# Optimization experiments

Hardware: AMD Instinct MI355X
Metric: run time of the kernel (lower is better)

Reference implementation:

```python
import jax, jax.numpy as jnp
import numpy as np

N = 4096      # num_nodes
F = 256       # node_dim
K = 4         # num_heads
FP = 64       # out_dim per head
P_EDGE = 0.008  # edge probability (~33 avg degree)


def setup_inputs() -> dict:
    key = jax.random.key(0)
    k1, k2, k3, k4, k5 = jax.random.split(key, 5)
    x = jax.random.normal(k1, (N, F), dtype=jnp.float32)
    # binary adjacency mask with self loops so every row has a neighbor
    adj = (jax.random.uniform(k2, (N, N)) < P_EDGE).astype(jnp.float32)
    mask = jnp.maximum(adj, jnp.eye(N, dtype=jnp.float32))
    batch = jnp.zeros((N,), dtype=jnp.int32)  # unused (is_final_layer=False)
    # xavier-style init for W (node_dim -> K*FP) and attention vectors
    w_scale = np.sqrt(2.0 / (F + K * FP)).astype(np.float32)
    W = jax.random.normal(k3, (F, K * FP), dtype=jnp.float32) * w_scale
    b = jnp.zeros((K * FP,), dtype=jnp.float32)
    a_scale = np.sqrt(2.0 / (K * FP + 1)).astype(np.float32)
    a_left = jax.random.normal(k4, (1, K, FP), dtype=jnp.float32) * a_scale
    a_right = jax.random.normal(k5, (1, K, FP), dtype=jnp.float32) * a_scale
    return {"x": x, "mask": mask, "batch": batch, "W": W, "b": b,
            "a_left": a_left, "a_right": a_right}


def reference(x, mask, batch, W, b, a_left, a_right):
    # dropout prob = 0.0 (eval mode) -> identity
    x_proj = (x @ W + b).reshape(N, K, FP)                 # (N,K,F')
    score_src = (x_proj * a_left).sum(axis=-1)             # (N,K)
    score_tgt = (x_proj * a_right).sum(axis=-1)            # (N,K)
    score = score_src[:, None, :] + score_tgt[None, :, :]  # (N,N,K)
    score = jax.nn.leaky_relu(score, negative_slope=0.2)
    # non-standard global mean/std normalization (torch .std() is unbiased)
    score = (score - score.mean()) / score.std(ddof=1)
    score = jnp.exp(score)
    m = mask[:, :, None]                                   # (N,N,1)
    denom = (score * m).sum(axis=1, keepdims=True)         # (N,1,K)
    aij = (score / denom) * m                              # (N,N,K)
    attention = jnp.transpose(aij, (2, 0, 1))              # (K,N,N)
    h_prime = jnp.einsum('knm,mkf->nkf', attention, x_proj)  # (N,K,F')
    h_prime = jax.nn.elu(h_prime)
    # is_final_layer=False -> concat heads
    return h_prime.reshape(N, K * FP)
```

## Files before the change

kernel.cpp:

```cpp
#include <hip/hip_runtime.h>
#include <hip/hip_bf16.h>
#include <math.h>

#define NN 4096
#define FF 256
#define KH 4
#define FP 64
#define NCOL 256
#define MAXNBR 512
#define MOM_BLOCKS 2048

__device__ __forceinline__ float bits2f(unsigned b) {
    union { unsigned u; float f; } c; c.u = b << 16; return c.f;
}
__device__ __forceinline__ int is_fp32(const void* mask) {
    return ((const unsigned*)mask)[0] == 0x3F800000u;
}

#define OFF_SUMS   0
#define OFF_PART   128
#define OFF_XP     65536
#define OFF_SRC    4259840
#define OFF_TGT    4325376

__global__ __launch_bounds__(256) void gat_gemm_valu(
        const void* __restrict__ xr, const void* __restrict__ mask,
        const void* __restrict__ Wr, const void* __restrict__ br,
        const void* __restrict__ alr, const void* __restrict__ arr,
        float* __restrict__ xp, float* __restrict__ src, float* __restrict__ tgt) {
    const int fl = is_fp32(mask);
    __shared__ float4 xs[8][64];
    int n0 = blockIdx.x * 8;
    if (fl) {
        const float4* xq = (const float4*)xr;
        for (int t = threadIdx.x; t < 512; t += 256) {
            int r = t >> 6, q = t & 63;
            xs[r][q] = xq[(size_t)(n0 + r) * 64 + q];
        }
    } else {
        const ushort4* xq = (const ushort4*)xr;
        for (int t = threadIdx.x; t < 512; t += 256) {
            int r = t >> 6, q = t & 63;
            ushort4 u = xq[(size_t)(n0 + r) * 64 + q];
            float4 v; v.x = bits2f(u.x); v.y = bits2f(u.y); v.z = bits2f(u.z); v.w = bits2f(u.w);
            xs[r][q] = v;
        }
    }
    __syncthreads();
    int c = threadIdx.x;
    float acc[8] = {};
    if (fl) {
        const float* WF = (const float*)Wr;
        for (int kk = 0; kk < 64; ++kk) {
            float w0 = WF[(4 * kk + 0) * NCOL + c];
            float w1 = WF[(4 * kk + 1) * NCOL + c];
            float w2 = WF[(4 * kk + 2) * NCOL + c];
            float w3 = WF[(4 * kk + 3) * NCOL + c];
            #pragma unroll
            for (int r = 0; r < 8; ++r) {
                float4 xv = xs[r][kk];
                acc[r] += xv.x * w0 + xv.y * w1 + xv.z * w2 + xv.w * w3;
            }
        }
    } else {
        const unsigned short* WB = (const unsigned short*)Wr;
        for (int kk = 0; kk < 64; ++kk) {
            float w0 = bits2f(WB[(4 * kk + 0) * NCOL + c]);
            float w1 = bits2f(WB[(4 * kk + 1) * NCOL + c]);
            float w2 = bits2f(WB[(4 * kk + 2) * NCOL + c]);
            float w3 = bits2f(WB[(4 * kk + 3) * NCOL + c]);
            #pragma unroll
            for (int r = 0; r < 8; ++r) {
                float4 xv = xs[r][kk];
                acc[r] += xv.x * w0 + xv.y * w1 + xv.z * w2 + xv.w * w3;
            }
        }
    }
    float bv, alv, arv;
    if (fl) {
        bv  = ((const float*)br)[c];
        alv = ((const float*)alr)[c];
        arv = ((const float*)arr)[c];
    } else {
        bv  = bits2f(((const unsigned short*)br)[c]);
        alv = bits2f(((const unsigned short*)alr)[c]);
        arv = bits2f(((const unsigned short*)arr)[c]);
    }
    int wave = threadIdx.x >> 6;
    int lane = threadIdx.x & 63;
    #pragma unroll
    for (int r = 0; r < 8; ++r) {
        float o = acc[r] + bv;
        xp[(size_t)(n0 + r) * NCOL + c] = o;
        float sr = o * alv, tr = o * arv;
        #pragma unroll
        for (int off = 32; off; off >>= 1) {
            sr += __shfl_down(sr, off, 64);
            tr += __shfl_down(tr, off, 64);
        }
        if (lane == 0) {
            src[(n0 + r) * KH + wave] = sr;
            tgt[(n0 + r) * KH + wave] = tr;
        }
    }
}

__global__ __launch_bounds__(256) void k_moments_a(
        const float* __restrict__ src, const float* __restrict__ tgt,
        double2* __restrict__ partials) {
    const int total = NN * NN;
    const int stride = MOM_BLOCKS * 256;
    float s1 = 0.f, s2 = 0.f;
    for (int p = blockIdx.x * 256 + threadIdx.x; p < total; p += stride) {
        int n = p >> 12, m = p & 4095;
        float4 sv = ((const float4*)src)[n];
        float4 tv = ((const float4*)tgt)[m];
        float v0 = sv.x + tv.x; v0 = v0 > 0.f ? v0 : 0.2f * v0;
        float v1 = sv.y + tv.y; v1 = v1 > 0.f ? v1 : 0.2f * v1;
        float v2 = sv.z + tv.z; v2 = v2 > 0.f ? v2 : 0.2f * v2;
        float v3 = sv.w + tv.w; v3 = v3 > 0.f ? v3 : 0.2f * v3;
        s1 += v0 + v1 + v2 + v3;
        s2 += v0 * v0 + v1 * v1 + v2 * v2 + v3 * v3;
    }
    __shared__ double l1[256], l2[256];
    l1[threadIdx.x] = (double)s1;
    l2[threadIdx.x] = (double)s2;
    __syncthreads();
    for (int off = 128; off; off >>= 1) {
        if (threadIdx.x < off) {
            l1[threadIdx.x] += l1[threadIdx.x + off];
            l2[threadIdx.x] += l2[threadIdx.x + off];
        }
        __syncthreads();
    }
    if (threadIdx.x == 0) {
        double2 pr; pr.x = l1[0]; pr.y = l2[0];
        partials[blockIdx.x] = pr;
    }
}

__global__ __launch_bounds__(256) void k_moments_b(
        const double2* __restrict__ partials, double* __restrict__ sums) {
    double a = 0.0, b = 0.0;
    for (int i = threadIdx.x; i < MOM_BLOCKS; i += 256) {
        double2 pr = partials[i];
        a += pr.x; b += pr.y;
    }
    __shared__ double l1[256], l2[256];
    l1[threadIdx.x] = a;
    l2[threadIdx.x] = b;
    __syncthreads();
    for (int off = 128; off; off >>= 1) {
        if (threadIdx.x < off) {
            l1[threadIdx.x] += l1[threadIdx.x + off];
            l2[threadIdx.x] += l2[threadIdx.x + off];
        }
        __syncthreads();
    }
    if (threadIdx.x == 0) {
        sums[0] = l1[0];
        sums[1] = l2[0];
    }
}

__global__ __launch_bounds__(256) void gat_aggregate(
        const void* __restrict__ mask,
        const float* __restrict__ xp,
        const float* __restrict__ src, const float* __restrict__ tgt,
        const double* __restrict__ sums,
        float* __restrict__ out) {
    __shared__ unsigned short snbr[MAXNBR];
    __shared__ float pls[MAXNBR * KH];
    __shared__ float invden[KH];
    __shared__ int cnt;
    const int fl = is_fp32(mask);
    int n = blockIdx.x;
    if (threadIdx.x == 0) cnt = 0;
    __syncthreads();

    if (fl) {
        const uint4* p = (const uint4*)((const float*)mask + (size_t)n * NN);
        for (int i = threadIdx.x; i < NN / 4; i += 256) {
            uint4 v = p[i]; int base = i * 4;
            if (v.x) { int s = atomicAdd(&cnt, 1); if (s < MAXNBR) snbr[s] = base + 0; }
            if (v.y) { int s = atomicAdd(&cnt, 1); if (s < MAXNBR) snbr[s] = base + 1; }
            if (v.z) { int s = atomicAdd(&cnt, 1); if (s < MAXNBR) snbr[s] = base + 2; }
            if (v.w) { int s = atomicAdd(&cnt, 1); if (s < MAXNBR) snbr[s] = base + 3; }
        }
    } else {
        const uint4* p = (const uint4*)((const unsigned short*)mask + (size_t)n * NN);
        for (int i = threadIdx.x; i < NN / 8; i += 256) {
            uint4 v = p[i]; int base = i * 8;
            if (v.x & 0xFFFFu) { int s = atomicAdd(&cnt, 1); if (s < MAXNBR) snbr[s] = base + 0; }
            if (v.x >> 16)     { int s = atomicAdd(&cnt, 1); if (s < MAXNBR) snbr[s] = base + 1; }
            if (v.y & 0xFFFFu) { int s = atomicAdd(&cnt, 1); if (s < MAXNBR) snbr[s] = base + 2; }
            if (v.y >> 16)     { int s = atomicAdd(&cnt, 1); if (s < MAXNBR) snbr[s] = base + 3; }
            if (v.z & 0xFFFFu) { int s = atomicAdd(&cnt, 1); if (s < MAXNBR) snbr[s] = base + 4; }
            if (v.z >> 16)     { int s = atomicAdd(&cnt, 1); if (s < MAXNBR) snbr[s] = base + 5; }
            if (v.w & 0xFFFFu) { int s = atomicAdd(&cnt, 1); if (s < MAXNBR) snbr[s] = base + 6; }
            if (v.w >> 16)     { int s = atomicAdd(&cnt, 1); if (s < MAXNBR) snbr[s] = base + 7; }
        }
    }
    __syncthreads();
    int c = cnt < MAXNBR ? cnt : MAXNBR;

    double s = sums[0], ss = sums[1];
    const double tot = (double)NN * (double)NN * (double)KH;
    float mu = (float)(s / tot);
    float inv_sigma = (float)(1.0 / sqrt((ss - s * s / tot) / (tot - 1.0)));

    for (int t = threadIdx.x; t < c * KH; t += 256) {
        int j = t >> 2, k = t & 3;
        int m = snbr[j];
        float v = src[n * KH + k] + tgt[m * KH + k];
        v = v > 0.f ? v : 0.2f * v;
        pls[j * KH + k] = expf((v - mu) * inv_sigma);
    }
    __syncthreads();
    if (threadIdx.x < KH) {
        float d = 0.f;
        for (int j = 0; j < c; ++j) d += pls[j * KH + threadIdx.x];
        invden[threadIdx.x] = 1.0f / d;
    }
    __syncthreads();

    int col = threadIdx.x;
    int k = col >> 6;
    float acc = 0.f;
    for (int j = 0; j < c; ++j) {
        acc += pls[j * KH + k] * xp[(size_t)snbr[j] * NCOL + col];
    }
    acc *= invden[k];
    float o = acc > 0.f ? acc : expm1f(acc);
    out[(size_t)n * NCOL + col] = o;
}

extern "C" void kernel_launch(void* const* d_in, const int* in_sizes, int n_in,
                              void* d_out, int out_size, void* d_ws, size_t ws_size,
                              hipStream_t stream) {
    const void* x    = d_in[0];
    const void* mask = d_in[1];
    const void* W    = d_in[3];
    const void* b    = d_in[4];
    const void* al   = d_in[5];
    const void* ar   = d_in[6];

    char* ws = (char*)d_ws;
    double* sums = (double*)(ws + OFF_SUMS);
    double2* part = (double2*)(ws + OFF_PART);
    float* xp   = (float*)(ws + OFF_XP);
    float* src  = (float*)(ws + OFF_SRC);
    float* tgt  = (float*)(ws + OFF_TGT);

    gat_gemm_valu<<<512, 256, 0, stream>>>(x, mask, W, b, al, ar, xp, src, tgt);
    k_moments_a<<<MOM_BLOCKS, 256, 0, stream>>>(src, tgt, part);
    k_moments_b<<<1, 256, 0, stream>>>(part, sums);
    gat_aggregate<<<4096, 256, 0, stream>>>(mask, xp, src, tgt, sums,
                                            (float*)d_out);
}
```

Measured before the change: 164.0 us.

## Fuse GEMM, moments, and aggregation into one cooperative kernel with grid syncs

The four launches (projection GEMM, two moment-reduction kernels, aggregation) become one cooperative kernel of 512 blocks separated by grid.sync. Each block now handles 8 rows of aggregation in sequence. Every block redundantly re-reduces the 512 partials to get mean and sigma. The moment pass is restructured so each thread holds one tgt entry and strides over src rows. This removes launch gaps and the separate final-reduction kernel, but aggregation parallelism drops from 4096 blocks to 512, and grid-wide barriers are added.

```diff
diff --git a/kernel.cpp b/kernel.cpp
--- a/kernel.cpp
+++ b/kernel.cpp
@@ -1,6 +1,9 @@
 #include <hip/hip_runtime.h>
 #include <hip/hip_bf16.h>
+#include <hip/hip_cooperative_groups.h>
 #include <math.h>
+
+namespace cg = cooperative_groups;
 
 #define NN 4096
 #define FF 256
@@ -8,7 +11,7 @@
 #define FP 64
 #define NCOL 256
 #define MAXNBR 512
-#define MOM_BLOCKS 2048
+#define NBLK 512
 
 __device__ __forceinline__ float bits2f(unsigned b) {
     union { unsigned u; float f; } c; c.u = b << 16; return c.f;
@@ -17,222 +20,223 @@
     return ((const unsigned*)mask)[0] == 0x3F800000u;
 }
 
-#define OFF_SUMS   0
-#define OFF_PART   128
+#define OFF_PART   0
 #define OFF_XP     65536
 #define OFF_SRC    4259840
 #define OFF_TGT    4325376
 
-__global__ __launch_bounds__(256) void gat_gemm_valu(
+__global__ __launch_bounds__(256) void gat_fused(
         const void* __restrict__ xr, const void* __restrict__ mask,
         const void* __restrict__ Wr, const void* __restrict__ br,
         const void* __restrict__ alr, const void* __restrict__ arr,
-        float* __restrict__ xp, float* __restrict__ src, float* __restrict__ tgt) {
+        float* __restrict__ xp, float* __restrict__ srcb, float* __restrict__ tgtb,
+        double2* __restrict__ partials, float* __restrict__ out) {
+    cg::grid_group grid = cg::this_grid();
     const int fl = is_fp32(mask);
-    __shared__ float4 xs[8][64];
-    int n0 = blockIdx.x * 8;
+    const int tid = threadIdx.x;
+    const int n0 = blockIdx.x * 8;
+
+    __shared__ union {
+        float4 xs[8][64];
+        struct { double l1[256], l2[256]; } red;
+        struct {
+            unsigned short snbr[MAXNBR];
+            float pls[MAXNBR * KH];
+            float invden[KH];
+            float musig[2];
+            int cnt;
+        } agg;
+    } sm;
+
     if (fl) {
         const float4* xq = (const float4*)xr;
-        for (int t = threadIdx.x; t < 512; t += 256) {
+        for (int t = tid; t < 512; t += 256) {
             int r = t >> 6, q = t & 63;
-            xs[r][q] = xq[(size_t)(n0 + r) * 64 + q];
+            sm.xs[r][q] = xq[(size_t)(n0 + r) * 64 + q];
         }
     } else {
         const ushort4* xq = (const ushort4*)xr;
-        for (int t = threadIdx.x; t < 512; t += 256) {
+        for (int t = tid; t < 512; t += 256) {
             int r = t >> 6, q = t & 63;
             ushort4 u = xq[(size_t)(n0 + r) * 64 + q];
             float4 v; v.x = bits2f(u.x); v.y = bits2f(u.y); v.z = bits2f(u.z); v.w = bits2f(u.w);
-            xs[r][q] = v;
+            sm.xs[r][q] = v;
         }
     }
     __syncthreads();
-    int c = threadIdx.x;
-    float acc[8] = {};
-    if (fl) {
-        const float* WF = (const float*)Wr;
-        for (int kk = 0; kk < 64; ++kk) {
-            float w0 = WF[(4 * kk + 0) * NCOL + c];
-            float w1 = WF[(4 * kk + 1) * NCOL + c];
-            float w2 = WF[(4 * kk + 2) * NCOL + c];
-            float w3 = WF[(4 * kk + 3) * NCOL + c];
+    {
+        int c = tid;
+        float acc[8] = {};
+        if (fl) {
+            const float* WF = (const float*)Wr;
+            for (int kk = 0; kk < 64; ++kk) {
+                float w0 = WF[(4 * kk + 0) * NCOL + c];
+                float w1 = WF[(4 * kk + 1) * NCOL + c];
+                float w2 = WF[(4 * kk + 2) * NCOL + c];
+                float w3 = WF[(4 * kk + 3) * NCOL + c];
+                #pragma unroll
+                for (int r = 0; r < 8; ++r) {
+                    float4 xv = sm.xs[r][kk];
+                    acc[r] += xv.x * w0 + xv.y * w1 + xv.z * w2 + xv.w * w3;
+                }
+            }
+        } else {
+            const unsigned short* WB = (const unsigned short*)Wr;
+            for (int kk = 0; kk < 64; ++kk) {
+                float w0 = bits2f(WB[(4 * kk + 0) * NCOL + c]);
+                float w1 = bits2f(WB[(4 * kk + 1) * NCOL + c]);
+                float w2 = bits2f(WB[(4 * kk + 2) * NCOL + c]);
+                float w3 = bits2f(WB[(4 * kk + 3) * NCOL + c]);
+                #pragma unroll
+                for (int r = 0; r < 8; ++r) {
+                    float4 xv = sm.xs[r][kk];
+                    acc[r] += xv.x * w0 + xv.y * w1 + xv.z * w2 + xv.w * w3;
+                }
+            }
+        }
+        float bv, alv, arv;
+        if (fl) {
+            bv  = ((const float*)br)[c];
+            alv = ((const float*)alr)[c];
+            arv = ((const float*)arr)[c];
+        } else {
+            bv  = bits2f(((const unsigned short*)br)[c]);
+            alv = bits2f(((const unsigned short*)alr)[c]);
+            arv = bits2f(((const unsigned short*)arr)[c]);
+        }
+        int wave = tid >> 6;
+        int lane = tid & 63;
+        #pragma unroll
+        for (int r = 0; r < 8; ++r) {
+            float o = acc[r] + bv;
+            xp[(size_t)(n0 + r) * NCOL + c] = o;
+            float sr = o * alv, tr = o * arv;
             #pragma unroll
-            for (int r = 0; r < 8; ++r) {
-                float4 xv = xs[r][kk];
-                acc[r] += xv.x * w0 + xv.y * w1 + xv.z * w2 + xv.w * w3;
-            }
-        }
-    } else {
-        const unsigned short* WB = (const unsigned short*)Wr;
-        for (int kk = 0; kk < 64; ++kk) {
-            float w0 = bits2f(WB[(4 * kk + 0) * NCOL + c]);
-            float w1 = bits2f(WB[(4 * kk + 1) * NCOL + c]);
-            float w2 = bits2f(WB[(4 * kk + 2) * NCOL + c]);
-            float w3 = bits2f(WB[(4 * kk + 3) * NCOL + c]);
-            #pragma unroll
-            for (int r = 0; r < 8; ++r) {
-                float4 xv = xs[r][kk];
-                acc[r] += xv.x * w0 + xv.y * w1 + xv.z * w2 + xv.w * w3;
-            }
-        }
-    }
-    float bv, alv, arv;
-    if (fl) {
-        bv  = ((const float*)br)[c];
-        alv = ((const float*)alr)[c];
-        arv = ((const float*)arr)[c];
-    } else {
-        bv  = bits2f(((const unsigned short*)br)[c]);
-        alv = bits2f(((const unsigned short*)alr)[c]);
-        arv = bits2f(((const unsigned short*)arr)[c]);
-    }
-    int wave = threadIdx.x >> 6;
-    int lane = threadIdx.x & 63;
-    #pragma unroll
+            for (int off = 32; off; off >>= 1) {
+                sr += __shfl_down(sr, off, 64);
+                tr += __shfl_down(tr, off, 64);
+            }
+            if (lane == 0) {
+                srcb[(n0 + r) * KH + wave] = sr;
+                tgtb[(n0 + r) * KH + wave] = tr;
+            }
+        }
+    }
+    grid.sync();
+
+    {
+        int id = blockIdx.x * 256 + tid;
+        int m = id & 4095;
+        int nb = id >> 12;
+        float4 tv = ((const float4*)tgtb)[m];
+        float s1 = 0.f, s2 = 0.f;
+        for (int n = nb; n < NN; n += 32) {
+            float4 sv = ((const float4*)srcb)[n];
+            float v0 = sv.x + tv.x; v0 = v0 > 0.f ? v0 : 0.2f * v0;
+            float v1 = sv.y + tv.y; v1 = v1 > 0.f ? v1 : 0.2f * v1;
+            float v2 = sv.z + tv.z; v2 = v2 > 0.f ? v2 : 0.2f * v2;
+            float v3 = sv.w + tv.w; v3 = v3 > 0.f ? v3 : 0.2f * v3;
+            s1 += v0 + v1 + v2 + v3;
+            s2 += v0 * v0 + v1 * v1 + v2 * v2 + v3 * v3;
+        }
+        __syncthreads();
+        sm.red.l1[tid] = (double)s1;
+        sm.red.l2[tid] = (double)s2;
+        __syncthreads();
+        for (int off = 128; off; off >>= 1) {
+            if (tid < off) {
+                sm.red.l1[tid] += sm.red.l1[tid + off];
+                sm.red.l2[tid] += sm.red.l2[tid + off];
+            }
+            __syncthreads();
+        }
+        if (tid == 0) {
+            double2 pr; pr.x = sm.red.l1[0]; pr.y = sm.red.l2[0];
+            partials[blockIdx.x] = pr;
+        }
+    }
+    grid.sync();
+
+    float mu, inv_sigma;
+    {
+        double a = 0.0, b2 = 0.0;
+        for (int i = tid; i < NBLK; i += 256) {
+            double2 pr = partials[i];
+            a += pr.x; b2 += pr.y;
+        }
+        sm.red.l1[tid] = a;
+        sm.red.l2[tid] = b2;
+        __syncthreads();
+        for (int off = 128; off; off >>= 1) {
+            if (tid < off) {
+                sm.red.l1[tid] += sm.red.l1[tid + off];
+                sm.red.l2[tid] += sm.red.l2[tid + off];
+            }
+            __syncthreads();
+        }
+        double s = sm.red.l1[0], ss = sm.red.l2[0];
+        const double tot = (double)NN * (double)NN * (double)KH;
+        mu = (float)(s / tot);
+        inv_sigma = (float)(1.0 / sqrt((ss - s * s / tot) / (tot - 1.0)));
+        __syncthreads();
+    }
+
     for (int r = 0; r < 8; ++r) {
-        float o = acc[r] + bv;
-        xp[(size_t)(n0 + r) * NCOL + c] = o;
-        float sr = o * alv, tr = o * arv;
-        #pragma unroll
-        for (int off = 32; off; off >>= 1) {
-            sr += __shfl_down(sr, off, 64);
-            tr += __shfl_down(tr, off, 64);
-        }
-        if (lane == 0) {
-            src[(n0 + r) * KH + wave] = sr;
-            tgt[(n0 + r) * KH + wave] = tr;
-        }
-    }
-}
-
-__global__ __launch_bounds__(256) void k_moments_a(
-        const float* __restrict__ src, const float* __restrict__ tgt,
-        double2* __restrict__ partials) {
-    const int total = NN * NN;
-    const int stride = MOM_BLOCKS * 256;
-    float s1 = 0.f, s2 = 0.f;
-    for (int p = blockIdx.x * 256 + threadIdx.x; p < total; p += stride) {
-        int n = p >> 12, m = p & 4095;
-        float4 sv = ((const float4*)src)[n];
-        float4 tv = ((const float4*)tgt)[m];
-        float v0 = sv.x + tv.x; v0 = v0 > 0.f ? v0 : 0.2f * v0;
-        float v1 = sv.y + tv.y; v1 = v1 > 0.f ? v1 : 0.2f * v1;
-        float v2 = sv.z + tv.z; v2 = v2 > 0.f ? v2 : 0.2f * v2;
-        float v3 = sv.w + tv.w; v3 = v3 > 0.f ? v3 : 0.2f * v3;
-        s1 += v0 + v1 + v2 + v3;
-        s2 += v0 * v0 + v1 * v1 + v2 * v2 + v3 * v3;
-    }
-    __shared__ double l1[256], l2[256];
-    l1[threadIdx.x] = (double)s1;
-    l2[threadIdx.x] = (double)s2;
-    __syncthreads();
-    for (int off = 128; off; off >>= 1) {
-        if (threadIdx.x < off) {
-            l1[threadIdx.x] += l1[threadIdx.x + off];
-            l2[threadIdx.x] += l2[threadIdx.x + off];
-        }
-        __syncthreads();
-    }
-    if (threadIdx.x == 0) {
-        double2 pr; pr.x = l1[0]; pr.y = l2[0];
-        partials[blockIdx.x] = pr;
-    }
-}
-
-__global__ __launch_bounds__(256) void k_moments_b(
-        const double2* __restrict__ partials, double* __restrict__ sums) {
-    double a = 0.0, b = 0.0;
-    for (int i = threadIdx.x; i < MOM_BLOCKS; i += 256) {
-        double2 pr = partials[i];
-        a += pr.x; b += pr.y;
-    }
-    __shared__ double l1[256], l2[256];
-    l1[threadIdx.x] = a;
-    l2[threadIdx.x] = b;
-    __syncthreads();
-    for (int off = 128; off; off >>= 1) {
-        if (threadIdx.x < off) {
-            l1[threadIdx.x] += l1[threadIdx.x + off];
-            l2[threadIdx.x] += l2[threadIdx.x + off];
-        }
-        __syncthreads();
-    }
-    if (threadIdx.x == 0) {
-        sums[0] = l1[0];
-        sums[1] = l2[0];
-    }
-}
-
-__global__ __launch_bounds__(256) void gat_aggregate(
-        const void* __restrict__ mask,
-        const float* __restrict__ xp,
-        const float* __restrict__ src, const float* __restrict__ tgt,
-        const double* __restrict__ sums,
-        float* __restrict__ out) {
-    __shared__ unsigned short snbr[MAXNBR];
-    __shared__ float pls[MAXNBR * KH];
-    __shared__ float invden[KH];
-    __shared__ int cnt;
-    const int fl = is_fp32(mask);
-    int n = blockIdx.x;
-    if (threadIdx.x == 0) cnt = 0;
-    __syncthreads();
-
-    if (fl) {
-        const uint4* p = (const uint4*)((const float*)mask + (size_t)n * NN);
-        for (int i = threadIdx.x; i < NN / 4; i += 256) {
-            uint4 v = p[i]; int base = i * 4;
-            if (v.x) { int s = atomicAdd(&cnt, 1); if (s < MAXNBR) snbr[s] = base + 0; }
-            if (v.y) { int s = atomicAdd(&cnt, 1); if (s < MAXNBR) snbr[s] = base + 1; }
-            if (v.z) { int s = atomicAdd(&cnt, 1); if (s < MAXNBR) snbr[s] = base + 2; }
-            if (v.w) { int s = atomicAdd(&cnt, 1); if (s < MAXNBR) snbr[s] = base + 3; }
-        }
-    } else {
-        const uint4* p = (const uint4*)((const unsigned short*)mask + (size_t)n * NN);
-        for (int i = threadIdx.x; i < NN / 8; i += 256) {
-            uint4 v = p[i]; int base = i * 8;
-            if (v.x & 0xFFFFu) { int s = atomicAdd(&cnt, 1); if (s < MAXNBR) snbr[s] = base + 0; }
-            if (v.x >> 16)     { int s = atomicAdd(&cnt, 1); if (s < MAXNBR) snbr[s] = base + 1; }
-            if (v.y & 0xFFFFu) { int s = atomicAdd(&cnt, 1); if (s < MAXNBR) snbr[s] = base + 2; }
-            if (v.y >> 16)     { int s = atomicAdd(&cnt, 1); if (s < MAXNBR) snbr[s] = base + 3; }
-            if (v.z & 0xFFFFu) { int s = atomicAdd(&cnt, 1); if (s < MAXNBR) snbr[s] = base + 4; }
-            if (v.z >> 16)     { int s = atomicAdd(&cnt, 1); if (s < MAXNBR) snbr[s] = base + 5; }
-            if (v.w & 0xFFFFu) { int s = atomicAdd(&cnt, 1); if (s < MAXNBR) snbr[s] = base + 6; }
-            if (v.w >> 16)     { int s = atomicAdd(&cnt, 1); if (s < MAXNBR) snbr[s] = base + 7; }
-        }
-    }
-    __syncthreads();
-    int c = cnt < MAXNBR ? cnt : MAXNBR;
-
-    double s = sums[0], ss = sums[1];
-    const double tot = (double)NN * (double)NN * (double)KH;
-    float mu = (float)(s / tot);
-    float inv_sigma = (float)(1.0 / sqrt((ss - s * s / tot) / (tot - 1.0)));
-
-    for (int t = threadIdx.x; t < c * KH; t += 256) {
-        int j = t >> 2, k = t & 3;
-        int m = snbr[j];
-        float v = src[n * KH + k] + tgt[m * KH + k];
-        v = v > 0.f ? v : 0.2f * v;
-        pls[j * KH + k] = expf((v - mu) * inv_sigma);
-    }
-    __syncthreads();
-    if (threadIdx.x < KH) {
-        float d = 0.f;
-        for (int j = 0; j < c; ++j) d += pls[j * KH + threadIdx.x];
-        invden[threadIdx.x] = 1.0f / d;
-    }
-    __syncthreads();
-
-    int col = threadIdx.x;
-    int k = col >> 6;
-    float acc = 0.f;
-    for (int j = 0; j < c; ++j) {
-        acc += pls[j * KH + k] * xp[(size_t)snbr[j] * NCOL + col];
-    }
-    acc *= invden[k];
-    float o = acc > 0.f ? acc : expm1f(acc);
-    out[(size_t)n * NCOL + col] = o;
+        int n = n0 + r;
+        if (tid == 0) sm.agg.cnt = 0;
+        __syncthreads();
+        if (fl) {
+            const uint4* p = (const uint4*)((const float*)mask + (size_t)n * NN);
+            for (int i = tid; i < NN / 4; i += 256) {
+                uint4 v = p[i]; int base = i * 4;
+                if (v.x) { int s = atomicAdd(&sm.agg.cnt, 1); if (s < MAXNBR) sm.agg.snbr[s] = base + 0; }
+                if (v.y) { int s = atomicAdd(&sm.agg.cnt, 1); if (s < MAXNBR) sm.agg.snbr[s] = base + 1; }
+                if (v.z) { int s = atomicAdd(&sm.agg.cnt, 1); if (s < MAXNBR) sm.agg.snbr[s] = base + 2; }
+                if (v.w) { int s = atomicAdd(&sm.agg.cnt, 1); if (s < MAXNBR) sm.agg.snbr[s] = base + 3; }
+            }
+        } else {
+            const uint4* p = (const uint4*)((const unsigned short*)mask + (size_t)n * NN);
+            for (int i = tid; i < NN / 8; i += 256) {
+                uint4 v = p[i]; int base = i * 8;
+                if (v.x & 0xFFFFu) { int s = atomicAdd(&sm.agg.cnt, 1); if (s < MAXNBR) sm.agg.snbr[s] = base + 0; }
+                if (v.x >> 16)     { int s = atomicAdd(&sm.agg.cnt, 1); if (s < MAXNBR) sm.agg.snbr[s] = base + 1; }
+                if (v.y & 0xFFFFu) { int s = atomicAdd(&sm.agg.cnt, 1); if (s < MAXNBR) sm.agg.snbr[s] = base + 2; }
+                if (v.y >> 16)     { int s = atomicAdd(&sm.agg.cnt, 1); if (s < MAXNBR) sm.agg.snbr[s] = base + 3; }
+                if (v.z & 0xFFFFu) { int s = atomicAdd(&sm.agg.cnt, 1); if (s < MAXNBR) sm.agg.snbr[s] = base + 4; }
+                if (v.z >> 16)     { int s = atomicAdd(&sm.agg.cnt, 1); if (s < MAXNBR) sm.agg.snbr[s] = base + 5; }
+                if (v.w & 0xFFFFu) { int s = atomicAdd(&sm.agg.cnt, 1); if (s < MAXNBR) sm.agg.snbr[s] = base + 6; }
+                if (v.w >> 16)     { int s = atomicAdd(&sm.agg.cnt, 1); if (s < MAXNBR) sm.agg.snbr[s] = base + 7; }
+            }
+        }
+        __syncthreads();
+        int c = sm.agg.cnt < MAXNBR ? sm.agg.cnt : MAXNBR;
+
+        for (int t = tid; t < c * KH; t += 256) {
+            int j = t >> 2, k = t & 3;
+            int m = sm.agg.snbr[j];
+            float v = srcb[n * KH + k] + tgtb[m * KH + k];
+            v = v > 0.f ? v : 0.2f * v;
+            sm.agg.pls[j * KH + k] = expf((v - mu) * inv_sigma);
+        }
+        __syncthreads();
+        if (tid < KH) {
+            float d = 0.f;
+            for (int j = 0; j < c; ++j) d += sm.agg.pls[j * KH + tid];
+            sm.agg.invden[tid] = 1.0f / d;
+        }
+        __syncthreads();
+
+        int col = tid;
+        int k = col >> 6;
+        float acc = 0.f;
+        for (int j = 0; j < c; ++j) {
+            acc += sm.agg.pls[j * KH + k] * xp[(size_t)sm.agg.snbr[j] * NCOL + col];
+        }
+        acc *= sm.agg.invden[k];
+        float o = acc > 0.f ? acc : expm1f(acc);
+        out[(size_t)n * NCOL + col] = o;
+        __syncthreads();
+    }
 }
 
 extern "C" void kernel_launch(void* const* d_in, const int* in_sizes, int n_in,
@@ -246,15 +250,15 @@
     const void* ar   = d_in[6];
 
     char* ws = (char*)d_ws;
-    double* sums = (double*)(ws + OFF_SUMS);
     double2* part = (double2*)(ws + OFF_PART);
     float* xp   = (float*)(ws + OFF_XP);
     float* src  = (float*)(ws + OFF_SRC);
     float* tgt  = (float*)(ws + OFF_TGT);
-
-    gat_gemm_valu<<<512, 256, 0, stream>>>(x, mask, W, b, al, ar, xp, src, tgt);
-    k_moments_a<<<MOM_BLOCKS, 256, 0, stream>>>(src, tgt, part);
-    k_moments_b<<<1, 256, 0, stream>>>(part, sums);
-    gat_aggregate<<<4096, 256, 0, stream>>>(mask, xp, src, tgt, sums,
-                                            (float*)d_out);
-}
+    float* outp = (float*)d_out;
+
+    void* args[] = { (void*)&x, (void*)&mask, (void*)&W, (void*)&b,
+                     (void*)&al, (void*)&ar, (void*)&xp, (void*)&src,
+                     (void*)&tgt, (void*)&part, (void*)&outp };
+    hipLaunchCooperativeKernel((const void*)gat_fused, dim3(NBLK), dim3(256),
+                               args, 0, stream);
+}
```

Result: slower. 323.8 us (+97.4%).
